# Kernel tuning notes

Hardware: AMD Instinct MI355X
Metric: run time of the kernel (lower is better)

## Reference

```python
import jax, jax.numpy as jnp
import numpy as np

NUM_CHOICES = 12
NUM_LAYERS = 32
LSTM_SIZE = 2048
TEMPERATURE = 5.0
TANH_CONSTANT = 2.5


def setup_inputs() -> dict:
    key = jax.random.key(0)
    ks = jax.random.split(key, 6)
    H, C = LSTM_SIZE, NUM_CHOICES
    u = lambda k, shape: jax.random.uniform(k, shape, jnp.float32, -0.1, 0.1)
    return {
        "prev_c": jnp.zeros((1, H), jnp.float32),
        "prev_h": jnp.zeros((1, H), jnp.float32),
        "encoder": u(ks[0], (C, H)),
        "w_ih": u(ks[1], (4 * H, H)),
        "w_hh": u(ks[2], (4 * H, H)),
        "b_ih": u(ks[3], (4 * H,)),
        "b_hh": u(ks[4], (4 * H,)),
        "w_soft": u(ks[5], (C, H)),
    }


def _rollout(prev_c, prev_h, encoder, w_ih, w_hh, b_ih, b_hh, w_soft):
    keys = jax.random.split(jax.random.key(42), NUM_LAYERS)
    x0 = encoder[0][None, :]  # inputs = encoder(zeros(1).long())

    def step(carry, key):
        c, h, x = carry
        # torch LSTMCell: gates = x W_ih^T + b_ih + h W_hh^T + b_hh; order i,f,g,o
        gates = x @ w_ih.T + b_ih + h @ w_hh.T + b_hh  # [1, 4H]
        i, f, g, o = jnp.split(gates, 4, axis=-1)
        c2 = jax.nn.sigmoid(f) * c + jax.nn.sigmoid(i) * jnp.tanh(g)
        h2 = jax.nn.sigmoid(o) * jnp.tanh(c2)
        logits = (h2 @ w_soft.T) / TEMPERATURE
        logits = TANH_CONSTANT * jnp.tanh(logits)  # [1, C]
        logp = jax.nn.log_softmax(logits, axis=-1)
        op = jax.random.categorical(key, logits[0])  # scalar int, ~ multinomial(prob,1)
        nll = -logp[0, op]  # F.cross_entropy(logits, op_id), batch=1
        ent = jax.lax.stop_gradient(-jnp.sum(jnp.exp(logp) * logp))
        x_next = encoder[op + 1][None, :]  # note: op+1 gather (clamped at table edge)
        return (c2, h2, x_next), (op, nll, ent)

    (_, _, _), (op_seq, nlls, ents) = jax.lax.scan(step, (prev_c, prev_h, x0), keys)
    return op_seq, jnp.sum(nlls), jnp.sum(ents)


def reference(prev_c, prev_h, encoder, w_ih, w_hh, b_ih, b_hh, w_soft):
    return _rollout(prev_c, prev_h, encoder, w_ih, w_hh, b_ih, b_hh, w_soft)
```

## Files before the change

### kernel.cpp

```cpp
#include <hip/hip_runtime.h>
#include <stdint.h>

#define HDIM 2048
#define NC   12
#define NL   32
#define NBLK 256
#define NTHR 512
#define NWAVE 8
#define FLAGMAGIC 0x600DF00Du
#define OPMAGIC   0xC0DE0000u
#define SPINCAP   2000000

__device__ __forceinline__ uint32_t rotl32(uint32_t x, int r) {
  return (x << r) | (x >> (32 - r));
}
__device__ __forceinline__ void tf2x32(uint32_t k0, uint32_t k1,
                                       uint32_t &x0, uint32_t &x1) {
  const uint32_t ks2 = k0 ^ k1 ^ 0x1BD11BDAu;
  x0 += k0; x1 += k1;
#define TFR(r) { x0 += x1; x1 = rotl32(x1, (r)); x1 ^= x0; }
  TFR(13) TFR(15) TFR(26) TFR(6)   x0 += k1;  x1 += ks2 + 1u;
  TFR(17) TFR(29) TFR(16) TFR(24)  x0 += ks2; x1 += k0  + 2u;
  TFR(13) TFR(15) TFR(26) TFR(6)   x0 += k0;  x1 += k1  + 3u;
  TFR(17) TFR(29) TFR(16) TFR(24)  x0 += k1;  x1 += ks2 + 4u;
  TFR(13) TFR(15) TFR(26) TFR(6)   x0 += ks2; x1 += k0  + 5u;
#undef TFR
}

__device__ __forceinline__ uint32_t ald(const uint32_t* p) {
  return __hip_atomic_load(p, __ATOMIC_RELAXED, __HIP_MEMORY_SCOPE_AGENT);
}
__device__ __forceinline__ void ast(uint32_t* p, uint32_t v) {
  __hip_atomic_store(p, v, __ATOMIC_RELAXED, __HIP_MEMORY_SCOPE_AGENT);
}
__device__ __forceinline__ float aldf(const float* p) {
  return __uint_as_float(__hip_atomic_load((const uint32_t*)p, __ATOMIC_RELAXED, __HIP_MEMORY_SCOPE_AGENT));
}
__device__ __forceinline__ void astf(float* p, float v) {
  __hip_atomic_store((uint32_t*)p, __float_as_uint(v), __ATOMIC_RELAXED, __HIP_MEMORY_SCOPE_AGENT);
}
__device__ __forceinline__ uint64_t ald64(const uint64_t* p) {
  return __hip_atomic_load(p, __ATOMIC_RELAXED, __HIP_MEMORY_SCOPE_AGENT);
}
#define VMCNT0() asm volatile("s_waitcnt vmcnt(0)" ::: "memory")
#define CFENCE() asm volatile("" ::: "memory")

__global__ void __launch_bounds__(NTHR, 2) ctrl_kernel(
    const float* __restrict__ prev_c, const float* __restrict__ prev_h,
    const float* __restrict__ encoder, const float* __restrict__ w_ih,
    const float* __restrict__ w_hh, const float* __restrict__ b_ih,
    const float* __restrict__ b_hh, const float* __restrict__ w_soft,
    float* __restrict__ out, float* __restrict__ ws)
{
  const int tid  = threadIdx.x;
  const int lane = tid & 63;
  const int wv   = tid >> 6;
  const int blk  = blockIdx.x;
  const int j    = blk * NWAVE + wv;

  float*    hbF    = ws;
  float*    partF  = ws + 2 * HDIM;
  uint32_t* flagsU = (uint32_t*)(ws + 2 * HDIM + 2 * NC * NBLK);
  uint32_t* opwU   = flagsU + NL * NBLK;

  __shared__ __align__(16) float s_h[HDIM];
  __shared__ float s_E[NWAVE][4][NC];
  __shared__ float s_part[NWAVE][NC];

  {
    float4 wif[4][8];
    #pragma unroll
    for (int g = 0; g < 4; ++g) {
      const float4* wp = reinterpret_cast<const float4*>(w_ih + (size_t)(g * HDIM + j) * HDIM);
      #pragma unroll
      for (int k = 0; k < 8; ++k) wif[g][k] = wp[k * 64 + lane];
    }
    float bsum[4];
    #pragma unroll
    for (int g = 0; g < 4; ++g) bsum[g] = b_ih[g * HDIM + j] + b_hh[g * HDIM + j];

    for (int c = 0; c < NC; ++c) {
      const float4* ep = reinterpret_cast<const float4*>(encoder + (size_t)c * HDIM);
      float s0 = 0.f, s1 = 0.f, s2 = 0.f, s3 = 0.f;
      #pragma unroll
      for (int k = 0; k < 8; ++k) {
        float4 e = ep[k * 64 + lane];
        s0 += wif[0][k].x*e.x + wif[0][k].y*e.y + wif[0][k].z*e.z + wif[0][k].w*e.w;
        s1 += wif[1][k].x*e.x + wif[1][k].y*e.y + wif[1][k].z*e.z + wif[1][k].w*e.w;
        s2 += wif[2][k].x*e.x + wif[2][k].y*e.y + wif[2][k].z*e.z + wif[2][k].w*e.w;
        s3 += wif[3][k].x*e.x + wif[3][k].y*e.y + wif[3][k].z*e.z + wif[3][k].w*e.w;
      }
      #pragma unroll
      for (int d = 1; d < 64; d <<= 1) {
        s0 += __shfl_xor(s0, d, 64); s1 += __shfl_xor(s1, d, 64);
        s2 += __shfl_xor(s2, d, 64); s3 += __shfl_xor(s3, d, 64);
      }
      if (lane == 0) {
        s_E[wv][0][c] = s0 + bsum[0]; s_E[wv][1][c] = s1 + bsum[1];
        s_E[wv][2][c] = s2 + bsum[2]; s_E[wv][3][c] = s3 + bsum[3];
      }
    }
  }
  __syncthreads();

  const float wsj = (lane < NC) ? w_soft[(size_t)lane * HDIM + j] : 0.f;
  float c_val   = prev_c[j];
  float nll_acc = 0.f, ent_acc = 0.f;

  for (int t = 0; t < NL; ++t) {
    if (t > 0) {
      if (wv == 0) {
        const uint32_t* f = flagsU + (size_t)(t - 1) * NBLK;
        for (int it = 0; it < SPINCAP; ++it) {
          uint32_t a0 = ald(f + lane), a1 = ald(f + lane + 64),
                   a2 = ald(f + lane + 128), a3 = ald(f + lane + 192);
          bool ok = (a0 == FLAGMAGIC) & (a1 == FLAGMAGIC) & (a2 == FLAGMAGIC) & (a3 == FLAGMAGIC);
          if (__all(ok)) break;
        }
        CFENCE();
      }
      __syncthreads();
      const uint64_t* hb64 = (const uint64_t*)(hbF + ((t - 1) & 1) * HDIM);
      ((uint64_t*)s_h)[2 * tid]     = ald64(hb64 + 2 * tid);
      ((uint64_t*)s_h)[2 * tid + 1] = ald64(hb64 + 2 * tid + 1);
    } else {
      reinterpret_cast<float4*>(s_h)[tid] = reinterpret_cast<const float4*>(prev_h)[tid];
    }
    __syncthreads();

    float4 hf[8];
    #pragma unroll
    for (int k = 0; k < 8; ++k) hf[k] = reinterpret_cast<const float4*>(s_h)[k * 64 + lane];

    float gate[4];
    #pragma unroll
    for (int g = 0; g < 4; ++g) {
      const float4* wp = reinterpret_cast<const float4*>(w_hh + (size_t)(g * HDIM + j) * HDIM);
      float s = 0.f;
      #pragma unroll
      for (int k = 0; k < 8; ++k) {
        float4 b = wp[k * 64 + lane];
        s += b.x*hf[k].x + b.y*hf[k].y + b.z*hf[k].z + b.w*hf[k].w;
      }
      #pragma unroll
      for (int d = 1; d < 64; d <<= 1) s += __shfl_xor(s, d, 64);
      gate[g] = s;
    }

    int c_idx = 0;
    if (t > 0) {
      uint32_t ow = 0;
      for (int it = 0; it < SPINCAP; ++it) {
        ow = ald(opwU + (t - 1));
        if ((ow & 0xFFFFFF00u) == OPMAGIC) break;
      }
      CFENCE();
      c_idx = (int)(ow & 0xFFu) + 1;
      if (c_idx > NC - 1) c_idx = NC - 1;
    }

    const float iv = 1.f / (1.f + expf(-(gate[0] + s_E[wv][0][c_idx])));
    const float fv = 1.f / (1.f + expf(-(gate[1] + s_E[wv][1][c_idx])));
    const float gv = tanhf(gate[2] + s_E[wv][2][c_idx]);
    const float ov = 1.f / (1.f + expf(-(gate[3] + s_E[wv][3][c_idx])));
    c_val = fv * c_val + iv * gv;
    const float h_new = ov * tanhf(c_val);

    if (lane == 0) astf(hbF + (t & 1) * HDIM + j, h_new);
    if (lane < NC) s_part[wv][lane] = h_new * wsj;
    VMCNT0();
    __syncthreads();
    if (wv == 0) {
      if (lane < NC) {
        float p = ((s_part[0][lane] + s_part[1][lane]) + (s_part[2][lane] + s_part[3][lane]))
                + ((s_part[4][lane] + s_part[5][lane]) + (s_part[6][lane] + s_part[7][lane]));
        astf(partF + (t & 1) * (NC * NBLK) + lane * NBLK + blk, p);
      }
      VMCNT0();
      if (lane == 0) ast(flagsU + (size_t)t * NBLK + blk, FLAGMAGIC);
    }

    if (blk == 0 && wv == 0) {
      {
        const uint32_t* f = flagsU + (size_t)t * NBLK;
        for (int it = 0; it < SPINCAP; ++it) {
          uint32_t a0 = ald(f + lane), a1 = ald(f + lane + 64),
                   a2 = ald(f + lane + 128), a3 = ald(f + lane + 192);
          bool ok = (a0 == FLAGMAGIC) & (a1 == FLAGMAGIC) & (a2 == FLAGMAGIC) & (a3 == FLAGMAGIC);
          if (__all(ok)) break;
        }
        CFENCE();
      }
      const float* pb = partF + (t & 1) * (NC * NBLK);
      float dot = 0.f;
      #pragma unroll
      for (int c = 0; c < NC; ++c) {
        float s = aldf(pb + c * NBLK + lane)       + aldf(pb + c * NBLK + lane + 64)
                + aldf(pb + c * NBLK + lane + 128) + aldf(pb + c * NBLK + lane + 192);
        #pragma unroll
        for (int d = 1; d < 64; d <<= 1) s += __shfl_xor(s, d, 64);
        if (lane == c) dot = s;
      }
      const float logit = 2.5f * tanhf(dot * 0.2f);

      uint32_t k0, k1, bits;
      { uint32_t a = 0u, b = (uint32_t)t;    tf2x32(0u, 42u, a, b); k0 = a; k1 = b; }
      { uint32_t a = 0u, b = (uint32_t)lane; tf2x32(k0, k1, a, b); bits = a ^ b; }
      const float TINY = 1.175494350822287508e-38f;
      float f01 = __uint_as_float((bits >> 9) | 0x3f800000u) - 1.0f;
      float u = f01 * (1.0f - TINY) + TINY;
      u = fmaxf(TINY, u);
      const float gmb = -logf(-logf(u));

      float by = (lane < NC) ? (logit + gmb) : -1e30f;
      int   bi = (lane < NC) ? lane : 999;
      #pragma unroll
      for (int d = 1; d < 16; d <<= 1) {
        float oy = __shfl_xor(by, d, 16);
        int   oi = __shfl_xor(bi, d, 16);
        if (oy > by || (oy == by && oi < bi)) { by = oy; bi = oi; }
      }
      const int op = bi;

      float m = (lane < NC) ? logit : -1e30f;
      #pragma unroll
      for (int d = 1; d < 16; d <<= 1) m = fmaxf(m, __shfl_xor(m, d, 16));
      const float sh = logit - m;
      float S = (lane < NC) ? expf(sh) : 0.f;
      #pragma unroll
      for (int d = 1; d < 16; d <<= 1) S += __shfl_xor(S, d, 16);
      const float lp = sh - logf(S);
      const float lp_op = __shfl(lp, op, 16);
      float tm = (lane < NC) ? expf(lp) * lp : 0.f;
      #pragma unroll
      for (int d = 1; d < 16; d <<= 1) tm += __shfl_xor(tm, d, 16);

      if (lane == 0) {
        out[t] = (float)op + 0.002f;
        nll_acc += -lp_op;
        ent_acc += -tm;
        ast(opwU + t, OPMAGIC | (uint32_t)op);
      }
    }
  }

  if (blk == 0 && tid == 0) { out[NL] = nll_acc; out[NL + 1] = ent_acc; }
}

extern "C" void kernel_launch(void* const* d_in, const int* in_sizes, int n_in,
                              void* d_out, int out_size, void* d_ws, size_t ws_size,
                              hipStream_t stream) {
  const float* prev_c  = (const float*)d_in[0];
  const float* prev_h  = (const float*)d_in[1];
  const float* encoder = (const float*)d_in[2];
  const float* w_ih    = (const float*)d_in[3];
  const float* w_hh    = (const float*)d_in[4];
  const float* b_ih    = (const float*)d_in[5];
  const float* b_hh    = (const float*)d_in[6];
  const float* w_soft  = (const float*)d_in[7];
  float* out = (float*)d_out;
  float* ws  = (float*)d_ws;

  void* args[] = {&prev_c, &prev_h, &encoder, &w_ih, &w_hh, &b_ih, &b_hh, &w_soft, &out, &ws};
  hipError_t e = hipLaunchCooperativeKernel(reinterpret_cast<void*>(ctrl_kernel),
                                            dim3(NBLK), dim3(NTHR), args, 0, stream);
  if (e != hipSuccess) {
    ctrl_kernel<<<dim3(NBLK), dim3(NTHR), 0, stream>>>(prev_c, prev_h, encoder, w_ih, w_hh,
                                                       b_ih, b_hh, w_soft, out, ws);
  }
}
```

Before: 650.7 us.

## Replicate sampling in every block to remove the op broadcast handoff

Each block now reads the previous step's partial logits after the barrier flag wait and runs the softmax and Gumbel sampling redundantly. This removes the serial chain where block 0 waited for all flags, sampled, and then published the op that every other block spun on. The cost is extra partial-sum loads and RNG work in every block, plus one more block-level barrier per step. The final step's sampling moves after the loop.

```diff
diff --git a/kernel.cpp b/kernel.cpp
--- a/kernel.cpp
+++ b/kernel.cpp
@@ -8,7 +8,6 @@
 #define NTHR 512
 #define NWAVE 8
 #define FLAGMAGIC 0x600DF00Du
-#define OPMAGIC   0xC0DE0000u
 #define SPINCAP   2000000
 
 __device__ __forceinline__ uint32_t rotl32(uint32_t x, int r) {
@@ -61,11 +60,11 @@
   float*    hbF    = ws;
   float*    partF  = ws + 2 * HDIM;
   uint32_t* flagsU = (uint32_t*)(ws + 2 * HDIM + 2 * NC * NBLK);
-  uint32_t* opwU   = flagsU + NL * NBLK;
 
   __shared__ __align__(16) float s_h[HDIM];
   __shared__ float s_E[NWAVE][4][NC];
   __shared__ float s_part[NWAVE][NC];
+  __shared__ int   s_op;
 
   {
     float4 wif[4][8];
@@ -108,6 +107,8 @@
   float nll_acc = 0.f, ent_acc = 0.f;
 
   for (int t = 0; t < NL; ++t) {
+    float pp0[NC], pp1[NC], pp2[NC], pp3[NC];
+
     if (t > 0) {
       if (wv == 0) {
         const uint32_t* f = flagsU + (size_t)(t - 1) * NBLK;
@@ -118,6 +119,14 @@
           if (__all(ok)) break;
         }
         CFENCE();
+        const float* pb = partF + ((t - 1) & 1) * (NC * NBLK);
+        #pragma unroll
+        for (int c = 0; c < NC; ++c) {
+          pp0[c] = aldf(pb + c * NBLK + lane);
+          pp1[c] = aldf(pb + c * NBLK + lane + 64);
+          pp2[c] = aldf(pb + c * NBLK + lane + 128);
+          pp3[c] = aldf(pb + c * NBLK + lane + 192);
+        }
       }
       __syncthreads();
       const uint64_t* hb64 = (const uint64_t*)(hbF + ((t - 1) & 1) * HDIM);
@@ -147,17 +156,60 @@
       gate[g] = s;
     }
 
-    int c_idx = 0;
-    if (t > 0) {
-      uint32_t ow = 0;
-      for (int it = 0; it < SPINCAP; ++it) {
-        ow = ald(opwU + (t - 1));
-        if ((ow & 0xFFFFFF00u) == OPMAGIC) break;
-      }
-      CFENCE();
-      c_idx = (int)(ow & 0xFFu) + 1;
-      if (c_idx > NC - 1) c_idx = NC - 1;
-    }
+    if (t > 0 && wv == 0) {
+      float dot = 0.f;
+      #pragma unroll
+      for (int c = 0; c < NC; ++c) {
+        float s = (pp0[c] + pp1[c]) + (pp2[c] + pp3[c]);
+        #pragma unroll
+        for (int d = 1; d < 64; d <<= 1) s += __shfl_xor(s, d, 64);
+        if (lane == c) dot = s;
+      }
+      const float logit = 2.5f * tanhf(dot * 0.2f);
+
+      uint32_t k0, k1, bits;
+      { uint32_t a = 0u, b = (uint32_t)(t - 1); tf2x32(0u, 42u, a, b); k0 = a; k1 = b; }
+      { uint32_t a = 0u, b = (uint32_t)lane;    tf2x32(k0, k1, a, b); bits = a ^ b; }
+      const float TINY = 1.175494350822287508e-38f;
+      float f01 = __uint_as_float((bits >> 9) | 0x3f800000u) - 1.0f;
+      float u = f01 * (1.0f - TINY) + TINY;
+      u = fmaxf(TINY, u);
+      const float gmb = -logf(-logf(u));
+
+      float by = (lane < NC) ? (logit + gmb) : -1e30f;
+      int   bi = (lane < NC) ? lane : 999;
+      #pragma unroll
+      for (int d = 1; d < 16; d <<= 1) {
+        float oy = __shfl_xor(by, d, 16);
+        int   oi = __shfl_xor(bi, d, 16);
+        if (oy > by || (oy == by && oi < bi)) { by = oy; bi = oi; }
+      }
+      const int op = bi;
+
+      if (blk == 0) {
+        float m = (lane < NC) ? logit : -1e30f;
+        #pragma unroll
+        for (int d = 1; d < 16; d <<= 1) m = fmaxf(m, __shfl_xor(m, d, 16));
+        const float sh = logit - m;
+        float S = (lane < NC) ? expf(sh) : 0.f;
+        #pragma unroll
+        for (int d = 1; d < 16; d <<= 1) S += __shfl_xor(S, d, 16);
+        const float lp = sh - logf(S);
+        const float lp_op = __shfl(lp, op, 16);
+        float tm = (lane < NC) ? expf(lp) * lp : 0.f;
+        #pragma unroll
+        for (int d = 1; d < 16; d <<= 1) tm += __shfl_xor(tm, d, 16);
+        if (lane == 0) {
+          out[t - 1] = (float)op + 0.002f;
+          nll_acc += -lp_op;
+          ent_acc += -tm;
+        }
+      }
+      if (lane == 0) s_op = op;
+    }
+    __syncthreads();
+
+    const int c_idx = (t == 0) ? 0 : ((s_op + 1 > NC - 1) ? NC - 1 : s_op + 1);
 
     const float iv = 1.f / (1.f + expf(-(gate[0] + s_E[wv][0][c_idx])));
     const float fv = 1.f / (1.f + expf(-(gate[1] + s_E[wv][1][c_idx])));
@@ -179,72 +231,69 @@
       VMCNT0();
       if (lane == 0) ast(flagsU + (size_t)t * NBLK + blk, FLAGMAGIC);
     }
-
-    if (blk == 0 && wv == 0) {
-      {
-        const uint32_t* f = flagsU + (size_t)t * NBLK;
-        for (int it = 0; it < SPINCAP; ++it) {
-          uint32_t a0 = ald(f + lane), a1 = ald(f + lane + 64),
-                   a2 = ald(f + lane + 128), a3 = ald(f + lane + 192);
-          bool ok = (a0 == FLAGMAGIC) & (a1 == FLAGMAGIC) & (a2 == FLAGMAGIC) & (a3 == FLAGMAGIC);
-          if (__all(ok)) break;
-        }
-        CFENCE();
-      }
-      const float* pb = partF + (t & 1) * (NC * NBLK);
-      float dot = 0.f;
-      #pragma unroll
-      for (int c = 0; c < NC; ++c) {
-        float s = aldf(pb + c * NBLK + lane)       + aldf(pb + c * NBLK + lane + 64)
-                + aldf(pb + c * NBLK + lane + 128) + aldf(pb + c * NBLK + lane + 192);
-        #pragma unroll
-        for (int d = 1; d < 64; d <<= 1) s += __shfl_xor(s, d, 64);
-        if (lane == c) dot = s;
-      }
-      const float logit = 2.5f * tanhf(dot * 0.2f);
-
-      uint32_t k0, k1, bits;
-      { uint32_t a = 0u, b = (uint32_t)t;    tf2x32(0u, 42u, a, b); k0 = a; k1 = b; }
-      { uint32_t a = 0u, b = (uint32_t)lane; tf2x32(k0, k1, a, b); bits = a ^ b; }
-      const float TINY = 1.175494350822287508e-38f;
-      float f01 = __uint_as_float((bits >> 9) | 0x3f800000u) - 1.0f;
-      float u = f01 * (1.0f - TINY) + TINY;
-      u = fmaxf(TINY, u);
-      const float gmb = -logf(-logf(u));
-
-      float by = (lane < NC) ? (logit + gmb) : -1e30f;
-      int   bi = (lane < NC) ? lane : 999;
-      #pragma unroll
-      for (int d = 1; d < 16; d <<= 1) {
-        float oy = __shfl_xor(by, d, 16);
-        int   oi = __shfl_xor(bi, d, 16);
-        if (oy > by || (oy == by && oi < bi)) { by = oy; bi = oi; }
-      }
-      const int op = bi;
-
-      float m = (lane < NC) ? logit : -1e30f;
-      #pragma unroll
-      for (int d = 1; d < 16; d <<= 1) m = fmaxf(m, __shfl_xor(m, d, 16));
-      const float sh = logit - m;
-      float S = (lane < NC) ? expf(sh) : 0.f;
-      #pragma unroll
-      for (int d = 1; d < 16; d <<= 1) S += __shfl_xor(S, d, 16);
-      const float lp = sh - logf(S);
-      const float lp_op = __shfl(lp, op, 16);
-      float tm = (lane < NC) ? expf(lp) * lp : 0.f;
-      #pragma unroll
-      for (int d = 1; d < 16; d <<= 1) tm += __shfl_xor(tm, d, 16);
-
-      if (lane == 0) {
-        out[t] = (float)op + 0.002f;
-        nll_acc += -lp_op;
-        ent_acc += -tm;
-        ast(opwU + t, OPMAGIC | (uint32_t)op);
-      }
-    }
   }
 
-  if (blk == 0 && tid == 0) { out[NL] = nll_acc; out[NL + 1] = ent_acc; }
+  if (blk == 0 && wv == 0) {
+    {
+      const uint32_t* f = flagsU + (size_t)(NL - 1) * NBLK;
+      for (int it = 0; it < SPINCAP; ++it) {
+        uint32_t a0 = ald(f + lane), a1 = ald(f + lane + 64),
+                 a2 = ald(f + lane + 128), a3 = ald(f + lane + 192);
+        bool ok = (a0 == FLAGMAGIC) & (a1 == FLAGMAGIC) & (a2 == FLAGMAGIC) & (a3 == FLAGMAGIC);
+        if (__all(ok)) break;
+      }
+      CFENCE();
+    }
+    const float* pb = partF + ((NL - 1) & 1) * (NC * NBLK);
+    float dot = 0.f;
+    #pragma unroll
+    for (int c = 0; c < NC; ++c) {
+      float s = (aldf(pb + c * NBLK + lane)       + aldf(pb + c * NBLK + lane + 64))
+              + (aldf(pb + c * NBLK + lane + 128) + aldf(pb + c * NBLK + lane + 192));
+      #pragma unroll
+      for (int d = 1; d < 64; d <<= 1) s += __shfl_xor(s, d, 64);
+      if (lane == c) dot = s;
+    }
+    const float logit = 2.5f * tanhf(dot * 0.2f);
+
+    uint32_t k0, k1, bits;
+    { uint32_t a = 0u, b = (uint32_t)(NL - 1); tf2x32(0u, 42u, a, b); k0 = a; k1 = b; }
+    { uint32_t a = 0u, b = (uint32_t)lane;     tf2x32(k0, k1, a, b); bits = a ^ b; }
+    const float TINY = 1.175494350822287508e-38f;
+    float f01 = __uint_as_float((bits >> 9) | 0x3f800000u) - 1.0f;
+    float u = f01 * (1.0f - TINY) + TINY;
+    u = fmaxf(TINY, u);
+    const float gmb = -logf(-logf(u));
+
+    float by = (lane < NC) ? (logit + gmb) : -1e30f;
+    int   bi = (lane < NC) ? lane : 999;
+    #pragma unroll
+    for (int d = 1; d < 16; d <<= 1) {
+      float oy = __shfl_xor(by, d, 16);
+      int   oi = __shfl_xor(bi, d, 16);
+      if (oy > by || (oy == by && oi < bi)) { by = oy; bi = oi; }
+    }
+    const int op = bi;
+
+    float m = (lane < NC) ? logit : -1e30f;
+    #pragma unroll
+    for (int d = 1; d < 16; d <<= 1) m = fmaxf(m, __shfl_xor(m, d, 16));
+    const float sh = logit - m;
+    float S = (lane < NC) ? expf(sh) : 0.f;
+    #pragma unroll
+    for (int d = 1; d < 16; d <<= 1) S += __shfl_xor(S, d, 16);
+    const float lp = sh - logf(S);
+    const float lp_op = __shfl(lp, op, 16);
+    float tm = (lane < NC) ? expf(lp) * lp : 0.f;
+    #pragma unroll
+    for (int d = 1; d < 16; d <<= 1) tm += __shfl_xor(tm, d, 16);
+
+    if (lane == 0) {
+      out[NL - 1] = (float)op + 0.002f;
+      out[NL]     = nll_acc + (-lp_op);
+      out[NL + 1] = ent_acc + (-tm);
+    }
+  }
 }
 
 extern "C" void kernel_launch(void* const* d_in, const int* in_sizes, int n_in,
```

Measured after the change: 828.4 us. +27.3%, slower.

## Replace flag barrier with tagged h writes and redundant per-block sampling

Applied to the files above, without the earlier changes.

Each block now publishes its h value packed with a step tag in one 64-bit word, and consumers spin directly on the tagged data instead of on separate per-block flags. Every block then recomputes the softmax logits and the Gumbel sample locally from the full h vector, instead of waiting for block 0 to reduce partial products and broadcast the chosen op. This removes a serialized global round trip per step (partials, flag, reduce, op broadcast) at the cost of redundant logit work and wider spin traffic in every block.

```diff
diff --git a/kernel.cpp b/kernel.cpp
--- a/kernel.cpp
+++ b/kernel.cpp
@@ -7,9 +7,8 @@
 #define NBLK 256
 #define NTHR 512
 #define NWAVE 8
-#define FLAGMAGIC 0x600DF00Du
-#define OPMAGIC   0xC0DE0000u
-#define SPINCAP   2000000
+#define SPINCAP 2000000
+#define TAG(t) (0x600D0000u | (uint32_t)(t))
 
 __device__ __forceinline__ uint32_t rotl32(uint32_t x, int r) {
   return (x << r) | (x >> (32 - r));
@@ -27,22 +26,12 @@
 #undef TFR
 }
 
-__device__ __forceinline__ uint32_t ald(const uint32_t* p) {
-  return __hip_atomic_load(p, __ATOMIC_RELAXED, __HIP_MEMORY_SCOPE_AGENT);
-}
-__device__ __forceinline__ void ast(uint32_t* p, uint32_t v) {
-  __hip_atomic_store(p, v, __ATOMIC_RELAXED, __HIP_MEMORY_SCOPE_AGENT);
-}
-__device__ __forceinline__ float aldf(const float* p) {
-  return __uint_as_float(__hip_atomic_load((const uint32_t*)p, __ATOMIC_RELAXED, __HIP_MEMORY_SCOPE_AGENT));
-}
-__device__ __forceinline__ void astf(float* p, float v) {
-  __hip_atomic_store((uint32_t*)p, __float_as_uint(v), __ATOMIC_RELAXED, __HIP_MEMORY_SCOPE_AGENT);
-}
 __device__ __forceinline__ uint64_t ald64(const uint64_t* p) {
   return __hip_atomic_load(p, __ATOMIC_RELAXED, __HIP_MEMORY_SCOPE_AGENT);
 }
-#define VMCNT0() asm volatile("s_waitcnt vmcnt(0)" ::: "memory")
+__device__ __forceinline__ void ast64(uint64_t* p, uint64_t v) {
+  __hip_atomic_store(p, v, __ATOMIC_RELAXED, __HIP_MEMORY_SCOPE_AGENT);
+}
 #define CFENCE() asm volatile("" ::: "memory")
 
 __global__ void __launch_bounds__(NTHR, 2) ctrl_kernel(
@@ -58,14 +47,14 @@
   const int blk  = blockIdx.x;
   const int j    = blk * NWAVE + wv;
 
-  float*    hbF    = ws;
-  float*    partF  = ws + 2 * HDIM;
-  uint32_t* flagsU = (uint32_t*)(ws + 2 * HDIM + 2 * NC * NBLK);
-  uint32_t* opwU   = flagsU + NL * NBLK;
+  uint64_t* hb = (uint64_t*)ws;
 
   __shared__ __align__(16) float s_h[HDIM];
   __shared__ float s_E[NWAVE][4][NC];
-  __shared__ float s_part[NWAVE][NC];
+  __shared__ float s_dot[16];
+  __shared__ int   s_op;
+
+  if (tid < 16) s_dot[tid] = 0.f;
 
   {
     float4 wif[4][8];
@@ -103,35 +92,109 @@
   }
   __syncthreads();
 
-  const float wsj = (lane < NC) ? w_soft[(size_t)lane * HDIM + j] : 0.f;
   float c_val   = prev_c[j];
   float nll_acc = 0.f, ent_acc = 0.f;
 
-  for (int t = 0; t < NL; ++t) {
+  for (int t = 0; t <= NL; ++t) {
+    if (t == 0) {
+      reinterpret_cast<float4*>(s_h)[tid] = reinterpret_cast<const float4*>(prev_h)[tid];
+    } else {
+      const uint64_t* base = hb + ((t - 1) & 1) * HDIM + wv * 256;
+      const uint32_t want = TAG(t - 1);
+      uint64_t v0 = 0, v1 = 0, v2 = 0, v3 = 0;
+      for (int it = 0; it < SPINCAP; ++it) {
+        v0 = ald64(base + lane);       v1 = ald64(base + lane + 64);
+        v2 = ald64(base + lane + 128); v3 = ald64(base + lane + 192);
+        bool ok = ((uint32_t)(v0 >> 32) == want) & ((uint32_t)(v1 >> 32) == want)
+                & ((uint32_t)(v2 >> 32) == want) & ((uint32_t)(v3 >> 32) == want);
+        if (__all(ok)) break;
+      }
+      CFENCE();
+      s_h[wv * 256 + lane]       = __uint_as_float((uint32_t)v0);
+      s_h[wv * 256 + lane + 64]  = __uint_as_float((uint32_t)v1);
+      s_h[wv * 256 + lane + 128] = __uint_as_float((uint32_t)v2);
+      s_h[wv * 256 + lane + 192] = __uint_as_float((uint32_t)v3);
+    }
+    __syncthreads();
+
     if (t > 0) {
-      if (wv == 0) {
-        const uint32_t* f = flagsU + (size_t)(t - 1) * NBLK;
-        for (int it = 0; it < SPINCAP; ++it) {
-          uint32_t a0 = ald(f + lane), a1 = ald(f + lane + 64),
-                   a2 = ald(f + lane + 128), a3 = ald(f + lane + 192);
-          bool ok = (a0 == FLAGMAGIC) & (a1 == FLAGMAGIC) & (a2 == FLAGMAGIC) & (a3 == FLAGMAGIC);
-          if (__all(ok)) break;
+      const int c0 = wv, c1 = wv + 8;
+      const float4* sh4 = reinterpret_cast<const float4*>(s_h);
+      const float4* wsA = reinterpret_cast<const float4*>(w_soft + (size_t)c0 * HDIM);
+      const float4* wsB = reinterpret_cast<const float4*>(w_soft + (size_t)(c1 < NC ? c1 : 0) * HDIM);
+      float d0 = 0.f, d1 = 0.f;
+      #pragma unroll
+      for (int k = 0; k < 8; ++k) {
+        float4 h4 = sh4[k * 64 + lane];
+        float4 a  = wsA[k * 64 + lane];
+        d0 += a.x*h4.x + a.y*h4.y + a.z*h4.z + a.w*h4.w;
+        if (c1 < NC) {
+          float4 b = wsB[k * 64 + lane];
+          d1 += b.x*h4.x + b.y*h4.y + b.z*h4.z + b.w*h4.w;
         }
-        CFENCE();
-      }
-      __syncthreads();
-      const uint64_t* hb64 = (const uint64_t*)(hbF + ((t - 1) & 1) * HDIM);
-      ((uint64_t*)s_h)[2 * tid]     = ald64(hb64 + 2 * tid);
-      ((uint64_t*)s_h)[2 * tid + 1] = ald64(hb64 + 2 * tid + 1);
-    } else {
-      reinterpret_cast<float4*>(s_h)[tid] = reinterpret_cast<const float4*>(prev_h)[tid];
+      }
+      #pragma unroll
+      for (int d = 1; d < 64; d <<= 1) {
+        d0 += __shfl_xor(d0, d, 64);
+        d1 += __shfl_xor(d1, d, 64);
+      }
+      if (lane == 0) {
+        s_dot[c0] = d0;
+        if (c1 < NC) s_dot[c1] = d1;
+      }
     }
     __syncthreads();
 
+    if (t > 0 && wv == 0) {
+      const int tt = t - 1;
+      const float logit = (lane < NC) ? 2.5f * tanhf(s_dot[lane] * 0.2f) : 0.f;
+
+      uint32_t k0, k1, bits;
+      { uint32_t a = 0u, b = (uint32_t)tt;   tf2x32(0u, 42u, a, b); k0 = a; k1 = b; }
+      { uint32_t a = 0u, b = (uint32_t)lane; tf2x32(k0, k1, a, b); bits = a ^ b; }
+      const float TINY = 1.175494350822287508e-38f;
+      float f01 = __uint_as_float((bits >> 9) | 0x3f800000u) - 1.0f;
+      float u = f01 * (1.0f - TINY) + TINY;
+      u = fmaxf(TINY, u);
+      const float gmb = -logf(-logf(u));
+
+      float by = (lane < NC) ? (logit + gmb) : -1e30f;
+      int   bi = (lane < NC) ? lane : 999;
+      #pragma unroll
+      for (int d = 1; d < 16; d <<= 1) {
+        float oy = __shfl_xor(by, d, 16);
+        int   oi = __shfl_xor(bi, d, 16);
+        if (oy > by || (oy == by && oi < bi)) { by = oy; bi = oi; }
+      }
+      const int op = bi;
+
+      if (blk == 0) {
+        float m = (lane < NC) ? logit : -1e30f;
+        #pragma unroll
+        for (int d = 1; d < 16; d <<= 1) m = fmaxf(m, __shfl_xor(m, d, 16));
+        const float sh = logit - m;
+        float S = (lane < NC) ? expf(sh) : 0.f;
+        #pragma unroll
+        for (int d = 1; d < 16; d <<= 1) S += __shfl_xor(S, d, 16);
+        const float lp = sh - logf(S);
+        const float lp_op = __shfl(lp, op, 16);
+        float tm = (lane < NC) ? expf(lp) * lp : 0.f;
+        #pragma unroll
+        for (int d = 1; d < 16; d <<= 1) tm += __shfl_xor(tm, d, 16);
+        if (lane == 0) {
+          out[tt] = (float)op + 0.002f;
+          nll_acc += -lp_op;
+          ent_acc += -tm;
+          if (t == NL) { out[NL] = nll_acc; out[NL + 1] = ent_acc; }
+        }
+      }
+      if (lane == 0) s_op = op;
+    }
+    if (t == NL) break;
+
     float4 hf[8];
     #pragma unroll
     for (int k = 0; k < 8; ++k) hf[k] = reinterpret_cast<const float4*>(s_h)[k * 64 + lane];
-
     float gate[4];
     #pragma unroll
     for (int g = 0; g < 4; ++g) {
@@ -146,18 +209,9 @@
       for (int d = 1; d < 64; d <<= 1) s += __shfl_xor(s, d, 64);
       gate[g] = s;
     }
-
-    int c_idx = 0;
-    if (t > 0) {
-      uint32_t ow = 0;
-      for (int it = 0; it < SPINCAP; ++it) {
-        ow = ald(opwU + (t - 1));
-        if ((ow & 0xFFFFFF00u) == OPMAGIC) break;
-      }
-      CFENCE();
-      c_idx = (int)(ow & 0xFFu) + 1;
-      if (c_idx > NC - 1) c_idx = NC - 1;
-    }
+    __syncthreads();
+
+    const int c_idx = (t == 0) ? 0 : ((s_op + 1 > NC - 1) ? NC - 1 : s_op + 1);
 
     const float iv = 1.f / (1.f + expf(-(gate[0] + s_E[wv][0][c_idx])));
     const float fv = 1.f / (1.f + expf(-(gate[1] + s_E[wv][1][c_idx])));
@@ -166,85 +220,11 @@
     c_val = fv * c_val + iv * gv;
     const float h_new = ov * tanhf(c_val);
 
-    if (lane == 0) astf(hbF + (t & 1) * HDIM + j, h_new);
-    if (lane < NC) s_part[wv][lane] = h_new * wsj;
-    VMCNT0();
-    __syncthreads();
-    if (wv == 0) {
-      if (lane < NC) {
-        float p = ((s_part[0][lane] + s_part[1][lane]) + (s_part[2][lane] + s_part[3][lane]))
-                + ((s_part[4][lane] + s_part[5][lane]) + (s_part[6][lane] + s_part[7][lane]));
-        astf(partF + (t & 1) * (NC * NBLK) + lane * NBLK + blk, p);
-      }
-      VMCNT0();
-      if (lane == 0) ast(flagsU + (size_t)t * NBLK + blk, FLAGMAGIC);
-    }
-
-    if (blk == 0 && wv == 0) {
-      {
-        const uint32_t* f = flagsU + (size_t)t * NBLK;
-        for (int it = 0; it < SPINCAP; ++it) {
-          uint32_t a0 = ald(f + lane), a1 = ald(f + lane + 64),
-                   a2 = ald(f + lane + 128), a3 = ald(f + lane + 192);
-          bool ok = (a0 == FLAGMAGIC) & (a1 == FLAGMAGIC) & (a2 == FLAGMAGIC) & (a3 == FLAGMAGIC);
-          if (__all(ok)) break;
-        }
-        CFENCE();
-      }
-      const float* pb = partF + (t & 1) * (NC * NBLK);
-      float dot = 0.f;
-      #pragma unroll
-      for (int c = 0; c < NC; ++c) {
-        float s = aldf(pb + c * NBLK + lane)       + aldf(pb + c * NBLK + lane + 64)
-                + aldf(pb + c * NBLK + lane + 128) + aldf(pb + c * NBLK + lane + 192);
-        #pragma unroll
-        for (int d = 1; d < 64; d <<= 1) s += __shfl_xor(s, d, 64);
-        if (lane == c) dot = s;
-      }
-      const float logit = 2.5f * tanhf(dot * 0.2f);
-
-      uint32_t k0, k1, bits;
-      { uint32_t a = 0u, b = (uint32_t)t;    tf2x32(0u, 42u, a, b); k0 = a; k1 = b; }
-      { uint32_t a = 0u, b = (uint32_t)lane; tf2x32(k0, k1, a, b); bits = a ^ b; }
-      const float TINY = 1.175494350822287508e-38f;
-      float f01 = __uint_as_float((bits >> 9) | 0x3f800000u) - 1.0f;
-      float u = f01 * (1.0f - TINY) + TINY;
-      u = fmaxf(TINY, u);
-      const float gmb = -logf(-logf(u));
-
-      float by = (lane < NC) ? (logit + gmb) : -1e30f;
-      int   bi = (lane < NC) ? lane : 999;
-      #pragma unroll
-      for (int d = 1; d < 16; d <<= 1) {
-        float oy = __shfl_xor(by, d, 16);
-        int   oi = __shfl_xor(bi, d, 16);
-        if (oy > by || (oy == by && oi < bi)) { by = oy; bi = oi; }
-      }
-      const int op = bi;
-
-      float m = (lane < NC) ? logit : -1e30f;
-      #pragma unroll
-      for (int d = 1; d < 16; d <<= 1) m = fmaxf(m, __shfl_xor(m, d, 16));
-      const float sh = logit - m;
-      float S = (lane < NC) ? expf(sh) : 0.f;
-      #pragma unroll
-      for (int d = 1; d < 16; d <<= 1) S += __shfl_xor(S, d, 16);
-      const float lp = sh - logf(S);
-      const float lp_op = __shfl(lp, op, 16);
-      float tm = (lane < NC) ? expf(lp) * lp : 0.f;
-      #pragma unroll
-      for (int d = 1; d < 16; d <<= 1) tm += __shfl_xor(tm, d, 16);
-
-      if (lane == 0) {
-        out[t] = (float)op + 0.002f;
-        nll_acc += -lp_op;
-        ent_acc += -tm;
-        ast(opwU + t, OPMAGIC | (uint32_t)op);
-      }
+    if (lane == 0) {
+      uint64_t w = ((uint64_t)TAG(t) << 32) | (uint64_t)__float_as_uint(h_new);
+      ast64(hb + (t & 1) * HDIM + j, w);
     }
   }
-
-  if (blk == 0 && tid == 0) { out[NL] = nll_acc; out[NL + 1] = ent_acc; }
 }
 
 extern "C" void kernel_launch(void* const* d_in, const int* in_sizes, int n_in,
```

New measurement: 765.5 us. +17.6%, slower.
